# Performance work log

Hardware: AMD Instinct MI355X
Metric: run time of the kernel (lower is better)

Reference implementation:

```python
import jax, jax.numpy as jnp
import numpy as np

DIM = 1024

def setup_inputs() -> dict:
    key = jax.random.key(0)
    ks = jax.random.split(key, 6)
    B, T, D = 8, 2048, DIM
    s = 1.0 / np.sqrt(D)
    x = jax.random.normal(ks[0], (B, T, D), dtype=jnp.float32)
    Wq = jax.random.normal(ks[1], (D, D), dtype=jnp.float32) * s
    Wk = jax.random.normal(ks[2], (D, D), dtype=jnp.float32) * s
    Wv = jax.random.normal(ks[3], (D, D), dtype=jnp.float32) * s
    Wp = jax.random.normal(ks[4], (D, D), dtype=jnp.float32) * s
    bp = jax.random.normal(ks[5], (D,), dtype=jnp.float32) * 0.01
    return {"x": x, "Wq": Wq, "Wk": Wk, "Wv": Wv, "Wp": Wp, "bp": bp}

def reference(x, Wq, Wk, Wv, Wp, bp):
    # x: [b, t, d]; weights stored as [d_in, d_out] (torch Linear applies x @ W.T;
    # here we bake the transpose into the stored matrix).
    scale = x.shape[-1] ** (-0.5)
    q = jnp.einsum('btd,de->bte', x, Wq)
    k = jnp.einsum('btd,de->bte', x, Wk)
    v = jnp.einsum('btd,de->bte', x, Wv)
    attn = jax.nn.softmax(jnp.einsum('btd,bTd->btT', q, k) * scale, axis=-1)
    out = jnp.einsum('btT,bTd->btd', attn, v)
    return jnp.einsum('btd,de->bte', out, Wp) + bp
```

## Files before the change

### kernel.cpp

```cpp
#include <hip/hip_runtime.h>


typedef _Float16 half_t;
typedef _Float16 half8 __attribute__((ext_vector_type(8)));
typedef float floatx4 __attribute__((ext_vector_type(4)));

#define GLD16(gp, lp)                                                          \
    __builtin_amdgcn_global_load_lds(                                          \
        (const __attribute__((address_space(1))) void*)(gp),                   \
        (__attribute__((address_space(3))) void*)(lp), 16, 0, 0)

#define WAIT_VM0()   asm volatile("s_waitcnt vmcnt(0)" ::: "memory")
#define WAIT_LGKM0() asm volatile("s_waitcnt lgkmcnt(0)" ::: "memory")
#define WAIT_LGKM8() asm volatile("s_waitcnt lgkmcnt(8)" ::: "memory")
#define BARRIER()   do { asm volatile("" ::: "memory");                        \
                         __builtin_amdgcn_s_barrier();                         \
                         asm volatile("" ::: "memory"); } while (0)

template<int EPI>
__global__ __launch_bounds__(512, 2)
void gemm16(const half_t* __restrict__ A, const half_t* __restrict__ B,
            void* __restrict__ Cv, void* __restrict__ C2, void* __restrict__ C3,
            const float* __restrict__ bias, int K, int lda, int ldb, int ldc,
            long long bsA, long long bsB, long long bsC)
{
    __shared__ half_t As[2 * 2 * 128 * 64];
    __shared__ half_t Bs[2 * 2 * 128 * 64];

    const int tid  = threadIdx.x;
    const int lane = tid & 63;
    const int w    = tid >> 6;
    const int wm   = w >> 2;
    const int wn   = w & 3;

    int bx = blockIdx.x, by = blockIdx.y, bz = blockIdx.z;
    {
        const int gx = gridDim.x, gy = gridDim.y;
        const int nwg = gx * gy * (int)gridDim.z;
        int lid = (bz * gy + by) * gx + bx;
        const int qq = nwg >> 3, rr = nwg & 7;
        const int xcd = lid & 7, off = lid >> 3;
        lid = (xcd < rr ? xcd * (qq + 1) : rr * (qq + 1) + (xcd - rr) * qq) + off;
        bx = lid % gx; lid /= gx;
        by = lid % gy; bz = lid / gy;
    }
    const long long z = bz;
    const int rowBase = by * 256;
    const int colBase = bx * 256;

    const int srow = lane >> 3;
    const int schk = (lane & 7) ^ srow;
    const half_t* gp[4];
    int jstep[4];
    half_t* lp[4];
    #pragma unroll
    for (int i = 0; i < 4; ++i) {
        const bool ia = (i < 2);
        const int ld  = ia ? lda : ldb;
        const int rb  = (ia ? rowBase : colBase) + (i & 1) * 128 + w * 16 + srow;
        gp[i] = (ia ? A + z * bsA : B + z * bsB) + (long long)rb * ld + schk * 8;
        jstep[i] = 8 * ld;
        lp[i] = (ia ? As : Bs) + (i & 1) * 8192 + w * 1024;
    }

    const int fr  = lane & 15;
    const int q   = lane >> 4;
    const int rsw = fr & 7;
    const half_t* Abase = As + wm * 8192 + fr * 64;
    const half_t* Bbase = Bs + (wn >> 1) * 8192 + ((wn & 1) * 64 + fr) * 64;
    const int ko0 = ((0 + q) ^ rsw) * 8;
    const int ko1 = ((4 + q) ^ rsw) * 8;

    floatx4 acc[8][4];
    #pragma unroll
    for (int m = 0; m < 8; ++m)
        #pragma unroll
        for (int n = 0; n < 4; ++n)
            #pragma unroll
            for (int j = 0; j < 4; ++j) acc[m][n][j] = 0.0f;

    const int nIter = K >> 6;

    #pragma unroll
    for (int i = 0; i < 4; ++i) {
        GLD16(gp[i],            lp[i]);
        GLD16(gp[i] + jstep[i], lp[i] + 512);
    }
    WAIT_VM0();
    BARRIER();

    for (int t = 0; t < nIter; ++t) {
        const int cbuf = (t & 1) << 14;
        const int nbuf = 16384 - cbuf;
        half8 bf[4][2], af[2][2];

        if (t + 1 < nIter) {
            const int kk = (t + 1) << 6;
            #pragma unroll
            for (int i = 0; i < 4; ++i) {
                GLD16(gp[i] + kk,            lp[i] + nbuf);
                GLD16(gp[i] + kk + jstep[i], lp[i] + nbuf + 512);
            }
        }
        #pragma unroll
        for (int n = 0; n < 4; ++n) {
            bf[n][0] = *(const half8*)(Bbase + cbuf + n * 1024 + ko0);
            bf[n][1] = *(const half8*)(Bbase + cbuf + n * 1024 + ko1);
        }
        af[0][0] = *(const half8*)(Abase + cbuf + 0 * 1024 + ko0);
        af[0][1] = *(const half8*)(Abase + cbuf + 0 * 1024 + ko1);
        af[1][0] = *(const half8*)(Abase + cbuf + 1 * 1024 + ko0);
        af[1][1] = *(const half8*)(Abase + cbuf + 1 * 1024 + ko1);
        WAIT_LGKM8();
        BARRIER();
        WAIT_LGKM0();
        __builtin_amdgcn_s_setprio(1);
        #pragma unroll
        for (int ml = 0; ml < 2; ++ml)
            #pragma unroll
            for (int n = 0; n < 4; ++n)
                #pragma unroll
                for (int ks = 0; ks < 2; ++ks)
                    acc[ml][n] = __builtin_amdgcn_mfma_f32_16x16x32_f16(
                        af[ml][ks], bf[n][ks], acc[ml][n], 0, 0, 0);
        __builtin_amdgcn_s_setprio(0);
        BARRIER();

        #pragma unroll
        for (int p = 1; p < 4; ++p) {
            #pragma unroll
            for (int ml = 0; ml < 2; ++ml) {
                af[ml][0] = *(const half8*)(Abase + cbuf + (p * 2 + ml) * 1024 + ko0);
                af[ml][1] = *(const half8*)(Abase + cbuf + (p * 2 + ml) * 1024 + ko1);
            }
            BARRIER();
            WAIT_LGKM0();
            __builtin_amdgcn_s_setprio(1);
            #pragma unroll
            for (int ml = 0; ml < 2; ++ml)
                #pragma unroll
                for (int n = 0; n < 4; ++n)
                    #pragma unroll
                    for (int ks = 0; ks < 2; ++ks)
                        acc[p * 2 + ml][n] = __builtin_amdgcn_mfma_f32_16x16x32_f16(
                            af[ml][ks], bf[n][ks], acc[p * 2 + ml][n], 0, 0, 0);
            __builtin_amdgcn_s_setprio(0);
            if (p == 3) WAIT_VM0();
            BARRIER();
        }
    }

    const int ecol = lane & 15;
    const int q4   = (lane >> 4) * 4;
    #pragma unroll
    for (int m = 0; m < 8; ++m) {
        #pragma unroll
        for (int n = 0; n < 4; ++n) {
            const int gcol = colBase + wn * 64 + n * 16 + ecol;
            #pragma unroll
            for (int r = 0; r < 4; ++r) {
                const int grow = rowBase + wm * 128 + m * 16 + q4 + r;
                float v = acc[m][n][r];
                if (EPI == 0) {
                    ((half_t*)Cv)[z * bsC + (long long)grow * ldc + gcol] = (half_t)v;
                } else if (EPI == 1) {
                    ((float*)Cv)[(long long)grow * ldc + gcol] = v + bias[gcol];
                } else {
                    const int mat = colBase >> 10;
                    const int c   = gcol & 1023;
                    if (mat == 0) {
                        ((half_t*)Cv)[(long long)grow * 1024 + c] = (half_t)(v * 0.03125f);
                    } else if (mat == 1) {
                        ((half_t*)C2)[(long long)grow * 1024 + c] = (half_t)v;
                    } else {
                        const long long bb = grow >> 11;
                        const long long tt = grow & 2047;
                        ((half_t*)C3)[bb * (1024LL * 2048) + (long long)c * 2048 + tt] = (half_t)v;
                    }
                }
            }
        }
    }
}

__global__ __launch_bounds__(256)
void cast16(const float* __restrict__ x, half_t* __restrict__ y)
{
    const long long i = ((long long)blockIdx.x * 256 + threadIdx.x) * 8;
    floatx4 a = *(const floatx4*)(x + i);
    floatx4 b = *(const floatx4*)(x + i + 4);
    half8 h;
    #pragma unroll
    for (int j = 0; j < 4; ++j) { h[j] = (half_t)a[j]; h[j + 4] = (half_t)b[j]; }
    *(half8*)(y + i) = h;
}

__global__ __launch_bounds__(256)
void cast_transpose4(const float* __restrict__ W0, const float* __restrict__ W1,
                     const float* __restrict__ W2, const float* __restrict__ W3,
                     half_t* __restrict__ WT)
{
    const float* W = (blockIdx.z == 0) ? W0 : (blockIdx.z == 1) ? W1
                   : (blockIdx.z == 2) ? W2 : W3;
    half_t* O = WT + (long long)blockIdx.z * 1024 * 1024;
    __shared__ float t[32][33];
    const int bx = blockIdx.x * 32, by = blockIdx.y * 32;
    const int tx = threadIdx.x, ty = threadIdx.y;
    #pragma unroll
    for (int i = 0; i < 32; i += 8)
        t[ty + i][tx] = W[(long long)(by + ty + i) * 1024 + bx + tx];
    __syncthreads();
    #pragma unroll
    for (int i = 0; i < 32; i += 8)
        O[(long long)(bx + ty + i) * 1024 + by + tx] = (half_t)t[tx][ty + i];
}

__global__ __launch_bounds__(256)
void softmax_rows(half_t* __restrict__ S)
{
    const long long base = (long long)blockIdx.x * 2048;
    const int t = threadIdx.x;
    half8 h = *(const half8*)(S + base + t * 8);
    float v[8];
    #pragma unroll
    for (int i = 0; i < 8; ++i) v[i] = (float)h[i];
    float m = -3.0e38f;
    #pragma unroll
    for (int i = 0; i < 8; ++i) m = fmaxf(m, v[i]);
    #pragma unroll
    for (int off = 32; off > 0; off >>= 1) m = fmaxf(m, __shfl_down(m, off));
    __shared__ float redm[4], reds[4];
    const int lane = t & 63, wid = t >> 6;
    if (lane == 0) redm[wid] = m;
    __syncthreads();
    const float M = fmaxf(fmaxf(redm[0], redm[1]), fmaxf(redm[2], redm[3]));
    float s = 0.f;
    #pragma unroll
    for (int i = 0; i < 8; ++i) { v[i] = __expf(v[i] - M); s += v[i]; }
    #pragma unroll
    for (int off = 32; off > 0; off >>= 1) s += __shfl_down(s, off);
    if (lane == 0) reds[wid] = s;
    __syncthreads();
    const float inv = 1.0f / (reds[0] + reds[1] + reds[2] + reds[3]);
    #pragma unroll
    for (int i = 0; i < 8; ++i) h[i] = (half_t)(v[i] * inv);
    *(half8*)(S + base + t * 8) = h;
}

extern "C" void kernel_launch(void* const* d_in, const int* in_sizes, int n_in,
                              void* d_out, int out_size, void* d_ws, size_t ws_size,
                              hipStream_t stream)
{
    const float* x  = (const float*)d_in[0];
    const float* Wq = (const float*)d_in[1];
    const float* Wk = (const float*)d_in[2];
    const float* Wv = (const float*)d_in[3];
    const float* Wp = (const float*)d_in[4];
    const float* bp = (const float*)d_in[5];
    float* out = (float*)d_out;

    char* ws = (char*)d_ws;
    const long long MB = 1024LL * 1024LL;
    half_t* WqkvT = (half_t*)(ws + 0 * MB);
    half_t* WpT   = (half_t*)(ws + 6 * MB);
    half_t* q     = (half_t*)(ws + 8 * MB);
    half_t* k     = (half_t*)(ws + 40 * MB);
    half_t* vT    = (half_t*)(ws + 72 * MB);
    half_t* x16   = (half_t*)(ws + 104 * MB);
    half_t* S     = (half_t*)(ws + 104 * MB);

    dim3 blk(512);
    cast16<<<8192, dim3(256), 0, stream>>>(x, x16);
    cast_transpose4<<<dim3(32, 32, 4), dim3(32, 8), 0, stream>>>(Wq, Wk, Wv, Wp, WqkvT);

    gemm16<2><<<dim3(12, 64, 1), blk, 0, stream>>>(
        x16, WqkvT, q, k, vT, nullptr, 1024, 1024, 1024, 0, 0, 0, 0);

    gemm16<0><<<dim3(8, 8, 8), blk, 0, stream>>>(
        q, k, S, nullptr, nullptr, nullptr, 1024, 1024, 1024, 2048,
        2048LL * 1024, 2048LL * 1024, 2048LL * 2048);

    softmax_rows<<<8 * 2048, dim3(256), 0, stream>>>(S);

    gemm16<0><<<dim3(4, 8, 8), blk, 0, stream>>>(
        S, vT, q, nullptr, nullptr, nullptr, 2048, 2048, 2048, 1024,
        2048LL * 2048, 1024LL * 2048, 2048LL * 1024);

    gemm16<1><<<dim3(4, 64, 1), blk, 0, stream>>>(
        q, WpT, out, nullptr, nullptr, bp, 1024, 1024, 1024, 1024, 0, 0, 0);
}
```

Measured before the change: 538.9 us.

## Double-buffer A fragments in registers and drop intra-iteration barriers

Restructures the GEMM main loop so A fragments are register double-buffered (afA/afB), with the LDS read of the next fragment issued before the MFMAs on the current one. The seven per-iteration barriers and explicit lgkmcnt waits are removed, leaving one vmcnt wait plus barrier per K-step. The aim is to cut synchronisation stalls and let LDS reads overlap MFMA work. In exchange it uses more VGPRs under launch_bounds(512,2), which may cause spills, and it relies on compiler-inserted waits for LDS reads.

```diff
diff --git a/kernel.cpp b/kernel.cpp
--- a/kernel.cpp
+++ b/kernel.cpp
@@ -10,9 +10,7 @@
         (const __attribute__((address_space(1))) void*)(gp),                   \
         (__attribute__((address_space(3))) void*)(lp), 16, 0, 0)
 
-#define WAIT_VM0()   asm volatile("s_waitcnt vmcnt(0)" ::: "memory")
-#define WAIT_LGKM0() asm volatile("s_waitcnt lgkmcnt(0)" ::: "memory")
-#define WAIT_LGKM8() asm volatile("s_waitcnt lgkmcnt(8)" ::: "memory")
+#define WAIT_VM0()  asm volatile("s_waitcnt vmcnt(0)" ::: "memory")
 #define BARRIER()   do { asm volatile("" ::: "memory");                        \
                          __builtin_amdgcn_s_barrier();                         \
                          asm volatile("" ::: "memory"); } while (0)
@@ -92,7 +90,17 @@
     for (int t = 0; t < nIter; ++t) {
         const int cbuf = (t & 1) << 14;
         const int nbuf = 16384 - cbuf;
-        half8 bf[4][2], af[2][2];
+        half8 bf[4][2], afA[2][2], afB[2][2];
+
+        #pragma unroll
+        for (int n = 0; n < 4; ++n) {
+            bf[n][0] = *(const half8*)(Bbase + cbuf + n * 1024 + ko0);
+            bf[n][1] = *(const half8*)(Bbase + cbuf + n * 1024 + ko1);
+        }
+        afA[0][0] = *(const half8*)(Abase + cbuf + 0 * 1024 + ko0);
+        afA[0][1] = *(const half8*)(Abase + cbuf + 0 * 1024 + ko1);
+        afA[1][0] = *(const half8*)(Abase + cbuf + 1 * 1024 + ko0);
+        afA[1][1] = *(const half8*)(Abase + cbuf + 1 * 1024 + ko1);
 
         if (t + 1 < nIter) {
             const int kk = (t + 1) << 6;
@@ -102,18 +110,12 @@
                 GLD16(gp[i] + kk + jstep[i], lp[i] + nbuf + 512);
             }
         }
-        #pragma unroll
-        for (int n = 0; n < 4; ++n) {
-            bf[n][0] = *(const half8*)(Bbase + cbuf + n * 1024 + ko0);
-            bf[n][1] = *(const half8*)(Bbase + cbuf + n * 1024 + ko1);
-        }
-        af[0][0] = *(const half8*)(Abase + cbuf + 0 * 1024 + ko0);
-        af[0][1] = *(const half8*)(Abase + cbuf + 0 * 1024 + ko1);
-        af[1][0] = *(const half8*)(Abase + cbuf + 1 * 1024 + ko0);
-        af[1][1] = *(const half8*)(Abase + cbuf + 1 * 1024 + ko1);
-        WAIT_LGKM8();
-        BARRIER();
-        WAIT_LGKM0();
+
+        afB[0][0] = *(const half8*)(Abase + cbuf + 2 * 1024 + ko0);
+        afB[0][1] = *(const half8*)(Abase + cbuf + 2 * 1024 + ko1);
+        afB[1][0] = *(const half8*)(Abase + cbuf + 3 * 1024 + ko0);
+        afB[1][1] = *(const half8*)(Abase + cbuf + 3 * 1024 + ko1);
+
         __builtin_amdgcn_s_setprio(1);
         #pragma unroll
         for (int ml = 0; ml < 2; ++ml)
@@ -122,32 +124,52 @@
                 #pragma unroll
                 for (int ks = 0; ks < 2; ++ks)
                     acc[ml][n] = __builtin_amdgcn_mfma_f32_16x16x32_f16(
-                        af[ml][ks], bf[n][ks], acc[ml][n], 0, 0, 0);
+                        afA[ml][ks], bf[n][ks], acc[ml][n], 0, 0, 0);
         __builtin_amdgcn_s_setprio(0);
+
+        afA[0][0] = *(const half8*)(Abase + cbuf + 4 * 1024 + ko0);
+        afA[0][1] = *(const half8*)(Abase + cbuf + 4 * 1024 + ko1);
+        afA[1][0] = *(const half8*)(Abase + cbuf + 5 * 1024 + ko0);
+        afA[1][1] = *(const half8*)(Abase + cbuf + 5 * 1024 + ko1);
+        __builtin_amdgcn_s_setprio(1);
+        #pragma unroll
+        for (int ml = 0; ml < 2; ++ml)
+            #pragma unroll
+            for (int n = 0; n < 4; ++n)
+                #pragma unroll
+                for (int ks = 0; ks < 2; ++ks)
+                    acc[2 + ml][n] = __builtin_amdgcn_mfma_f32_16x16x32_f16(
+                        afB[ml][ks], bf[n][ks], acc[2 + ml][n], 0, 0, 0);
+        __builtin_amdgcn_s_setprio(0);
+
+        afB[0][0] = *(const half8*)(Abase + cbuf + 6 * 1024 + ko0);
+        afB[0][1] = *(const half8*)(Abase + cbuf + 6 * 1024 + ko1);
+        afB[1][0] = *(const half8*)(Abase + cbuf + 7 * 1024 + ko0);
+        afB[1][1] = *(const half8*)(Abase + cbuf + 7 * 1024 + ko1);
+        __builtin_amdgcn_s_setprio(1);
+        #pragma unroll
+        for (int ml = 0; ml < 2; ++ml)
+            #pragma unroll
+            for (int n = 0; n < 4; ++n)
+                #pragma unroll
+                for (int ks = 0; ks < 2; ++ks)
+                    acc[4 + ml][n] = __builtin_amdgcn_mfma_f32_16x16x32_f16(
+                        afA[ml][ks], bf[n][ks], acc[4 + ml][n], 0, 0, 0);
+        __builtin_amdgcn_s_setprio(0);
+
+        __builtin_amdgcn_s_setprio(1);
+        #pragma unroll
+        for (int ml = 0; ml < 2; ++ml)
+            #pragma unroll
+            for (int n = 0; n < 4; ++n)
+                #pragma unroll
+                for (int ks = 0; ks < 2; ++ks)
+                    acc[6 + ml][n] = __builtin_amdgcn_mfma_f32_16x16x32_f16(
+                        afB[ml][ks], bf[n][ks], acc[6 + ml][n], 0, 0, 0);
+        __builtin_amdgcn_s_setprio(0);
+
+        WAIT_VM0();
         BARRIER();
-
-        #pragma unroll
-        for (int p = 1; p < 4; ++p) {
-            #pragma unroll
-            for (int ml = 0; ml < 2; ++ml) {
-                af[ml][0] = *(const half8*)(Abase + cbuf + (p * 2 + ml) * 1024 + ko0);
-                af[ml][1] = *(const half8*)(Abase + cbuf + (p * 2 + ml) * 1024 + ko1);
-            }
-            BARRIER();
-            WAIT_LGKM0();
-            __builtin_amdgcn_s_setprio(1);
-            #pragma unroll
-            for (int ml = 0; ml < 2; ++ml)
-                #pragma unroll
-                for (int n = 0; n < 4; ++n)
-                    #pragma unroll
-                    for (int ks = 0; ks < 2; ++ks)
-                        acc[p * 2 + ml][n] = __builtin_amdgcn_mfma_f32_16x16x32_f16(
-                            af[ml][ks], bf[n][ks], acc[p * 2 + ml][n], 0, 0, 0);
-            __builtin_amdgcn_s_setprio(0);
-            if (p == 3) WAIT_VM0();
-            BARRIER();
-        }
     }
 
     const int ecol = lane & 15;
```

Result: faster. 490.4 us (-9.0%).
